# Kernel optimization log

Measured on AMD Instinct MI355X. Metric: run time of the kernel, lower is better.

The kernel has to match this reference:

```python
import jax, jax.numpy as jnp
import numpy as np

NP, P, H, NB = 14, 16, 12, 6  # n_patches per side, patch size, heads, blocks
HD, EMB, SEQ = 64, 768, NP * NP + 1


def _layernorm(x, g, b, eps=1e-5):
    m = x.mean(axis=-1, keepdims=True)
    v = x.var(axis=-1, keepdims=True)
    return (x - m) * jax.lax.rsqrt(v + eps) * g + b


def setup_inputs() -> dict:
    key = jax.random.key(0)
    ks = jax.random.split(key, 16)
    s = 0.02
    B = 64
    inp = {
        "images": jax.random.normal(ks[0], (B, 3, 224, 224), jnp.float32),
        "Wmap": jax.random.normal(ks[1], (768, 768), jnp.float32) * s,
        "bmap": jnp.zeros((768,), jnp.float32),
        "cls_tok": jax.random.normal(ks[2], (1, 768), jnp.float32) * s,
        "pos": jax.random.normal(ks[3], (SEQ, 768), jnp.float32) * s,
        "ln1_g": jnp.ones((NB, 768), jnp.float32),
        "ln1_b": jnp.zeros((NB, 768), jnp.float32),
        "Wq": jax.random.normal(ks[4], (NB, H, HD, HD), jnp.float32) * s,
        "bq": jnp.zeros((NB, H, HD), jnp.float32),
        "Wk": jax.random.normal(ks[5], (NB, H, HD, HD), jnp.float32) * s,
        "bk": jnp.zeros((NB, H, HD), jnp.float32),
        "Wv": jax.random.normal(ks[6], (NB, H, HD, HD), jnp.float32) * s,
        "bv": jnp.zeros((NB, H, HD), jnp.float32),
        "ln2_g": jnp.ones((NB, 768), jnp.float32),
        "ln2_b": jnp.zeros((NB, 768), jnp.float32),
        "W1": jax.random.normal(ks[7], (NB, 768, 3072), jnp.float32) * s,
        "b1": jnp.zeros((NB, 3072), jnp.float32),
        "W2": jax.random.normal(ks[8], (NB, 3072, 768), jnp.float32) * s,
        "b2": jnp.zeros((NB, 768), jnp.float32),
        "Whead": jax.random.normal(ks[9], (768, 10), jnp.float32) * s,
        "bhead": jnp.zeros((10,), jnp.float32),
    }
    return inp


def reference(images, Wmap, bmap, cls_tok, pos, ln1_g, ln1_b, Wq, bq, Wk, bk,
              Wv, bv, ln2_g, ln2_b, W1, b1, W2, b2, Whead, bhead):
    B = images.shape[0]
    # patchify: (B,3,224,224) -> (B,196,768); per-patch channel-first flatten
    x = images.reshape(B, 3, NP, P, NP, P)
    x = x.transpose(0, 2, 4, 1, 3, 5).reshape(B, NP * NP, 3 * P * P)
    tokens = x @ Wmap + bmap  # (B,196,768)
    tokens = jnp.concatenate(
        [jnp.broadcast_to(cls_tok[None], (B, 1, EMB)), tokens], axis=1)
    out = tokens + pos[None]  # (B,197,768)
    scale = 1.0 / jnp.sqrt(jnp.asarray(H, out.dtype))  # NOTE: source divides by sqrt(num_heads)
    for i in range(NB):
        h = _layernorm(out, ln1_g[i], ln1_b[i])
        xh = h.reshape(B, SEQ, H, HD)
        q = jnp.einsum('bshd,hde->bshe', xh, Wq[i]) + bq[i]
        k = jnp.einsum('bshd,hde->bshe', xh, Wk[i]) + bk[i]
        v = jnp.einsum('bshd,hde->bshe', xh, Wv[i]) + bv[i]
        attn = jax.nn.softmax(
            jnp.einsum('bqhd,bkhd->bhqk', q, k) * scale, axis=-1)
        o = jnp.einsum('bhqk,bkhd->bqhd', attn, v).reshape(B, SEQ, EMB)
        out = out + o
        h2 = _layernorm(out, ln2_g[i], ln2_b[i])
        mlp = jax.nn.gelu(h2 @ W1[i] + b1[i], approximate=False) @ W2[i] + b2[i]
        out = out + mlp
    cls = out[:, 0]  # (B,768)
    return jax.nn.softmax(cls @ Whead + bhead, axis=-1)
```

## Files before the change

kernel.cpp:

```cpp
#include <hip/hip_runtime.h>
#include <cstddef>

#define BATCH 64
#define SEQL  197
#define EMB   768
#define NH    12
#define HDIM  64
#define NBLK  6
#define MLPD  3072
#define TOKS  12608
#define PTOK  12544
#define ATT_SCALE 0.28867513459481287f
#define LOG2E 1.4426950408889634f

typedef short bf16x8 __attribute__((ext_vector_type(8)));
typedef float f32x4  __attribute__((ext_vector_type(4)));

__device__ inline float bf2f(unsigned short u) {
  union { unsigned int i; float f; } c; c.i = ((unsigned int)u) << 16; return c.f;
}
__device__ inline unsigned short f2bf(float f) {
  union { float f; unsigned int i; } c; c.f = f;
  unsigned int r = c.i + 0x7FFFu + ((c.i >> 16) & 1u);
  return (unsigned short)(r >> 16);
}

__device__ __forceinline__ float gelu_f(float x) {
  float u = __builtin_fabsf(x) * 0.70710678118654752f;
  float t = __builtin_amdgcn_rcpf(__builtin_fmaf(0.3275911f, u, 1.0f));
  float p = __builtin_fmaf(1.061405429f, t, -1.453152027f);
  p = __builtin_fmaf(p, t, 1.421413741f);
  p = __builtin_fmaf(p, t, -0.284496736f);
  p = __builtin_fmaf(p, t, 0.254829592f);
  p = p * t;
  float e = __expf(-u * u);
  float er = __builtin_fmaf(-p, e, 1.0f);
  er = __builtin_copysignf(er, x);
  return 0.5f * x * (1.0f + er);
}

__device__ __forceinline__ void gload16(const unsigned short* g, void* l) {
  __builtin_amdgcn_global_load_lds(
      (const __attribute__((address_space(1))) unsigned int*)g,
      (__attribute__((address_space(3))) unsigned int*)l, 16, 0, 0);
}

__global__ __launch_bounds__(256) void patchify_kernel(const float* __restrict__ img,
                                                       unsigned short* __restrict__ out) {
  int i4 = blockIdx.x * 256 + threadIdx.x;
  int f4 = i4 % 192;
  int r  = i4 / 192;
  int b  = r / 196, t = r - b * 196;
  int f  = f4 * 4;
  int c  = f >> 8;
  int rem = f & 255;
  int iy = rem >> 4, ix = rem & 15;
  int py = t / 14, px = t - py * 14;
  const float* src = img + ((((size_t)b * 3 + c) * 224 + py * 16 + iy) * 224 + px * 16 + ix);
  float4 v = *(const float4*)src;
  ushort4 u;
  u.x = f2bf(v.x); u.y = f2bf(v.y); u.z = f2bf(v.z); u.w = f2bf(v.w);
  *(ushort4*)(out + (size_t)r * 768 + f) = u;
}

__global__ __launch_bounds__(256) void clspos_kernel(const float* __restrict__ cls,
                                                     const float* __restrict__ pos,
                                                     float* __restrict__ X) {
  int idx = blockIdx.x * 256 + threadIdx.x;
  int b = idx / 768, e = idx - b * 768;
  X[(size_t)b * SEQL * 768 + e] = cls[e] + pos[e];
}

__global__ __launch_bounds__(256) void wconv_kernel(const float* __restrict__ W,
                                                    unsigned short* __restrict__ Wt,
                                                    int K, int N, int perm) {
  __shared__ float t[32][33];
  int k0 = blockIdx.x * 32, n0 = blockIdx.y * 32;
  int kk = threadIdx.x >> 3, nn = (threadIdx.x & 7) * 4;
  float4 v = *(const float4*)&W[(size_t)(k0 + kk) * N + n0 + nn];
  t[nn + 0][kk] = v.x; t[nn + 1][kk] = v.y; t[nn + 2][kk] = v.z; t[nn + 3][kk] = v.w;
  __syncthreads();
  int nr = threadIdx.x >> 3, kc = (threadIdx.x & 7) * 4;
  ushort4 u;
  u.x = f2bf(t[nr][kc + 0]); u.y = f2bf(t[nr][kc + 1]);
  u.z = f2bf(t[nr][kc + 2]); u.w = f2bf(t[nr][kc + 3]);
  if (!perm) {
    *(ushort4*)&Wt[(size_t)(n0 + nr) * K + k0 + kc] = u;
  } else {
    size_t base = (size_t)(n0 + nr) * K + (size_t)(k0 & ~63);
    int klo = (k0 & 32) + kc;
    size_t st = base + (size_t)((klo & 15) * 4 + (klo >> 4));
    Wt[st + 0]  = u.x;
    Wt[st + 4]  = u.y;
    Wt[st + 8]  = u.z;
    Wt[st + 12] = u.w;
  }
}

__global__ __launch_bounds__(256) void qwconv_kernel(const float* __restrict__ Wq,
                                                     const float* __restrict__ Wk,
                                                     const float* __restrict__ Wv,
                                                     unsigned short* __restrict__ Wt) {
  int mh = blockIdx.x;
  int m = mh / 12, h = mh - m * 12;
  const float* src = (m == 0 ? Wq : (m == 1 ? Wk : Wv)) + (size_t)h * 4096;
  unsigned short* dst = Wt + (size_t)mh * 4096;
  for (int idx = threadIdx.x; idx < 4096; idx += 256) {
    int d = idx >> 6, e = idx & 63;
    dst[e * 64 + d] = f2bf(src[idx]);
  }
}

template<int MODE>
__global__ __launch_bounds__(256) void gemm_mfma(const unsigned short* __restrict__ A, int lda,
                                                 const unsigned short* __restrict__ Bt, int ldb,
                                                 void* __restrict__ Cv,
                                                 const float* __restrict__ bias,
                                                 const float* __restrict__ pos,
                                                 int M, int N, int K) {
  __shared__ short As[8192];
  __shared__ short Bs[8192];
  const int tid  = threadIdx.x;
  const int wid  = tid >> 6, lane = tid & 63;
  const int wr   = wid >> 1, wc = wid & 1;
  const int fr   = lane & 15;
  const int fq   = lane >> 4;
  const int m0   = blockIdx.y * 128;
  const int n0   = blockIdx.x * 128;
  const int srow = lane >> 3;
  const int schk = lane & 7;
  const int Mc   = M - 1;

  f32x4 acc[4][4];
#pragma unroll
  for (int m = 0; m < 4; ++m)
#pragma unroll
    for (int n = 0; n < 4; ++n) acc[m][n] = (f32x4)0.f;

  for (int k0 = 0; k0 < K; k0 += 64) {
#pragma unroll
    for (int i = 0; i < 4; ++i) {
      int row = i * 32 + wid * 8 + srow;
      int gr = m0 + row; if (gr > Mc) gr = Mc;
      gload16(A + (size_t)gr * lda + k0 + ((schk ^ (row & 7)) << 3),
              (char*)As + i * 4096 + wid * 1024);
      gload16(Bt + (size_t)(n0 + row) * ldb + k0 + ((schk ^ (row & 7)) << 3),
              (char*)Bs + i * 4096 + wid * 1024);
    }
    __syncthreads();
#pragma unroll
    for (int ks = 0; ks < 2; ++ks) {
      bf16x8 af[4], bfr[4];
#pragma unroll
      for (int m = 0; m < 4; ++m) {
        int row = (wr << 6) + (m << 4) + fr;
        int ch = ((ks << 2) + fq) ^ (row & 7);
        af[m] = *(const bf16x8*)&As[(row << 6) + (ch << 3)];
      }
#pragma unroll
      for (int n = 0; n < 4; ++n) {
        int row = (wc << 6) + (n << 4) + fr;
        int ch = ((ks << 2) + fq) ^ (row & 7);
        bfr[n] = *(const bf16x8*)&Bs[(row << 6) + (ch << 3)];
      }
#pragma unroll
      for (int m = 0; m < 4; ++m)
#pragma unroll
        for (int n = 0; n < 4; ++n)
          acc[m][n] = __builtin_amdgcn_mfma_f32_16x16x32_bf16(af[m], bfr[n], acc[m][n], 0, 0, 0);
    }
    __syncthreads();
  }

#pragma unroll
  for (int m = 0; m < 4; ++m) {
#pragma unroll
    for (int j = 0; j < 4; ++j) {
      int r = m0 + (wr << 6) + (m << 4) + (fq << 2) + j;
      if (r >= M) continue;
      if (MODE == 1) {
        ushort4 q;
        float v0 = acc[m][0][j] + bias[n0 + (wc << 6) + 0 * 16 + fr];
        float v1 = acc[m][1][j] + bias[n0 + (wc << 6) + 1 * 16 + fr];
        float v2 = acc[m][2][j] + bias[n0 + (wc << 6) + 2 * 16 + fr];
        float v3 = acc[m][3][j] + bias[n0 + (wc << 6) + 3 * 16 + fr];
        q.x = f2bf(gelu_f(v0));
        q.y = f2bf(gelu_f(v1));
        q.z = f2bf(gelu_f(v2));
        q.w = f2bf(gelu_f(v3));
        *(ushort4*)&((unsigned short*)Cv)[(size_t)r * MLPD + n0 + (wc << 6) + fr * 4] = q;
      } else {
#pragma unroll
        for (int n = 0; n < 4; ++n) {
          int c = n0 + (wc << 6) + (n << 4) + fr;
          float v = acc[m][n][j] + bias[c];
          if (MODE == 0) {
            int b = r / 196, t = r - b * 196;
            ((float*)Cv)[((size_t)b * SEQL + 1 + t) * 768 + c] = v + pos[(size_t)(1 + t) * 768 + c];
          } else {
            ((float*)Cv)[(size_t)r * 768 + c] += v;
          }
        }
      }
    }
  }
}

__global__ __launch_bounds__(256) void ln_kernel(const float* __restrict__ Xi,
                                                 unsigned short* __restrict__ Ho,
                                                 const float* __restrict__ g,
                                                 const float* __restrict__ bb) {
  int tok = blockIdx.x * 4 + (threadIdx.x >> 6);
  int lane = threadIdx.x & 63;
  const float* x = Xi + (size_t)tok * 768;
  float4 v0 = *(const float4*)(x + lane * 4);
  float4 v1 = *(const float4*)(x + 256 + lane * 4);
  float4 v2 = *(const float4*)(x + 512 + lane * 4);
  float s = v0.x + v0.y + v0.z + v0.w + v1.x + v1.y + v1.z + v1.w + v2.x + v2.y + v2.z + v2.w;
  float q = v0.x*v0.x + v0.y*v0.y + v0.z*v0.z + v0.w*v0.w
          + v1.x*v1.x + v1.y*v1.y + v1.z*v1.z + v1.w*v1.w
          + v2.x*v2.x + v2.y*v2.y + v2.z*v2.z + v2.w*v2.w;
#pragma unroll
  for (int o = 32; o > 0; o >>= 1) { s += __shfl_xor(s, o); q += __shfl_xor(q, o); }
  float mean = s * (1.f / 768.f);
  float var  = q * (1.f / 768.f) - mean * mean;
  float rs = rsqrtf(var + 1e-5f);
  unsigned short* outp = Ho + (size_t)tok * 768;
  float4 g0 = *(const float4*)(g + lane * 4);
  float4 g1 = *(const float4*)(g + 256 + lane * 4);
  float4 g2 = *(const float4*)(g + 512 + lane * 4);
  float4 b0 = *(const float4*)(bb + lane * 4);
  float4 b1 = *(const float4*)(bb + 256 + lane * 4);
  float4 b2 = *(const float4*)(bb + 512 + lane * 4);
  ushort4 s0, s1, s2;
  s0.x = f2bf((v0.x - mean) * rs * g0.x + b0.x); s0.y = f2bf((v0.y - mean) * rs * g0.y + b0.y);
  s0.z = f2bf((v0.z - mean) * rs * g0.z + b0.z); s0.w = f2bf((v0.w - mean) * rs * g0.w + b0.w);
  s1.x = f2bf((v1.x - mean) * rs * g1.x + b1.x); s1.y = f2bf((v1.y - mean) * rs * g1.y + b1.y);
  s1.z = f2bf((v1.z - mean) * rs * g1.z + b1.z); s1.w = f2bf((v1.w - mean) * rs * g1.w + b1.w);
  s2.x = f2bf((v2.x - mean) * rs * g2.x + b2.x); s2.y = f2bf((v2.y - mean) * rs * g2.y + b2.y);
  s2.z = f2bf((v2.z - mean) * rs * g2.z + b2.z); s2.w = f2bf((v2.w - mean) * rs * g2.w + b2.w);
  *(ushort4*)(outp + lane * 4) = s0;
  *(ushort4*)(outp + 256 + lane * 4) = s1;
  *(ushort4*)(outp + 512 + lane * 4) = s2;
}

__global__ __launch_bounds__(256) void qkv_mfma(const unsigned short* __restrict__ Hb,
    const unsigned short* __restrict__ Wt,
    const float* __restrict__ bq, const float* __restrict__ bk, const float* __restrict__ bv,
    unsigned short* __restrict__ Qo, unsigned short* __restrict__ Ko,
    unsigned short* __restrict__ Vo) {
  const int h = blockIdx.y;
  const int tid = threadIdx.x, wv = tid >> 6, lane = tid & 63;
  const int fr = lane & 15, hi = lane >> 4;
  const int t0 = blockIdx.x * 64 + wv * 16;
  const unsigned short* arow = Hb + (size_t)(t0 + fr) * 768 + h * 64;
  bf16x8 a0 = *(const bf16x8*)(arow + hi * 8);
  bf16x8 a1 = *(const bf16x8*)(arow + 32 + hi * 8);
  f32x4 acc[3][4];
#pragma unroll
  for (int m = 0; m < 3; ++m)
#pragma unroll
    for (int n = 0; n < 4; ++n) acc[m][n] = (f32x4)0.f;
#pragma unroll
  for (int m = 0; m < 3; ++m) {
    const unsigned short* wb = Wt + (size_t)(m * 12 + h) * 4096;
#pragma unroll
    for (int n = 0; n < 4; ++n) {
      bf16x8 b0 = *(const bf16x8*)&wb[(n * 16 + fr) * 64 + hi * 8];
      bf16x8 b1 = *(const bf16x8*)&wb[(n * 16 + fr) * 64 + 32 + hi * 8];
      acc[m][n] = __builtin_amdgcn_mfma_f32_16x16x32_bf16(a0, b0, acc[m][n], 0, 0, 0);
      acc[m][n] = __builtin_amdgcn_mfma_f32_16x16x32_bf16(a1, b1, acc[m][n], 0, 0, 0);
    }
  }
#pragma unroll
  for (int m = 0; m < 3; ++m) {
    const float* bptr = (m == 0 ? bq : (m == 1 ? bk : bv)) + h * 64;
    unsigned short* optr = (m == 0 ? Qo : (m == 1 ? Ko : Vo));
    const float sc = (m == 0) ? ATT_SCALE : 1.f;
#pragma unroll
    for (int j = 0; j < 4; ++j) {
      int tk = t0 + hi * 4 + j;
      int b = tk / 197, s = tk - b * 197;
      size_t base_o = (((size_t)b * NH + h) * SEQL + s) * 64;
      if (m < 2) {
        ushort4 o;
        o.x = f2bf((acc[m][0][j] + bptr[0 * 16 + fr]) * sc);
        o.y = f2bf((acc[m][1][j] + bptr[1 * 16 + fr]) * sc);
        o.z = f2bf((acc[m][2][j] + bptr[2 * 16 + fr]) * sc);
        o.w = f2bf((acc[m][3][j] + bptr[3 * 16 + fr]) * sc);
        *(ushort4*)&optr[base_o + fr * 4] = o;
      } else {
#pragma unroll
        for (int n = 0; n < 4; ++n)
          optr[base_o + n * 16 + fr] = f2bf(acc[m][n][j] + bptr[n * 16 + fr]);
      }
    }
  }
}

__global__ __launch_bounds__(256) void attn_kernel(const unsigned short* __restrict__ Q,
                                                   const unsigned short* __restrict__ Kg,
                                                   const unsigned short* __restrict__ Vg,
                                                   float* __restrict__ X) {
  __shared__ unsigned short Vt[64][200];
  __shared__ unsigned short Pl[4][16][200];
  const int bh = blockIdx.x;
  const int b = bh / NH, h = bh - b * NH;
  const int tid = threadIdx.x, wv = tid >> 6, lane = tid & 63;
  const int fr = lane & 15, hi = lane >> 4;
  const unsigned short* Qp = Q  + (size_t)bh * SEQL * 64;
  const unsigned short* Kp = Kg + (size_t)bh * SEQL * 64;
  const unsigned short* Vp = Vg + (size_t)bh * SEQL * 64;

  for (int idx = tid; idx < SEQL * 16; idx += 256) {
    int s = idx >> 4, d4 = (idx & 15) * 4;
    ushort4 v = *(const ushort4*)&Vp[s * 64 + d4];
    Vt[d4 + 0][s] = v.x; Vt[d4 + 1][s] = v.y; Vt[d4 + 2][s] = v.z; Vt[d4 + 3][s] = v.w;
  }
  __syncthreads();

  for (int qt = wv; qt < 13; qt += 4) {
    int qrow = qt * 16 + fr; if (qrow > 196) qrow = 196;
    bf16x8 qa0 = *(const bf16x8*)&Qp[qrow * 64 + hi * 8];
    bf16x8 qa1 = *(const bf16x8*)&Qp[qrow * 64 + 32 + hi * 8];
    f32x4 sc[13];
#pragma unroll
    for (int kt = 0; kt < 13; ++kt) {
      int krow = kt * 16 + fr; if (krow > 196) krow = 196;
      bf16x8 kb0 = *(const bf16x8*)&Kp[krow * 64 + hi * 8];
      bf16x8 kb1 = *(const bf16x8*)&Kp[krow * 64 + 32 + hi * 8];
      f32x4 a = (f32x4)0.f;
      __builtin_amdgcn_s_setprio(1);
      a = __builtin_amdgcn_mfma_f32_16x16x32_bf16(qa0, kb0, a, 0, 0, 0);
      a = __builtin_amdgcn_mfma_f32_16x16x32_bf16(qa1, kb1, a, 0, 0, 0);
      __builtin_amdgcn_s_setprio(0);
      sc[kt] = a;
    }
    float mx[4] = {-3e38f, -3e38f, -3e38f, -3e38f};
#pragma unroll
    for (int kt = 0; kt < 13; ++kt) {
      bool inval = (kt == 12) && (fr >= 5);
#pragma unroll
      for (int j = 0; j < 4; ++j) {
        float s = inval ? -3e38f : sc[kt][j];
        sc[kt][j] = s;
        mx[j] = fmaxf(mx[j], s);
      }
    }
#pragma unroll
    for (int o = 8; o > 0; o >>= 1)
#pragma unroll
      for (int j = 0; j < 4; ++j) mx[j] = fmaxf(mx[j], __shfl_xor(mx[j], o));
    float l[4] = {0.f, 0.f, 0.f, 0.f};
#pragma unroll
    for (int kt = 0; kt < 13; ++kt) {
      int col = kt * 16 + fr;
      bool storev = (col < 200);
#pragma unroll
      for (int j = 0; j < 4; ++j) {
        float p = exp2f((sc[kt][j] - mx[j]) * LOG2E);
        if ((kt == 12) && (fr >= 5)) p = 0.f;
        l[j] += p;
        if (storev) Pl[wv][hi * 4 + j][col] = f2bf(p);
      }
    }
#pragma unroll
    for (int o = 8; o > 0; o >>= 1)
#pragma unroll
      for (int j = 0; j < 4; ++j) l[j] += __shfl_xor(l[j], o);
    f32x4 ov[4];
#pragma unroll
    for (int n = 0; n < 4; ++n) ov[n] = (f32x4)0.f;
#pragma unroll
    for (int kc = 0; kc < 6; ++kc) {
      bf16x8 pa = *(const bf16x8*)&Pl[wv][fr][kc * 32 + hi * 8];
      __builtin_amdgcn_s_setprio(1);
#pragma unroll
      for (int n = 0; n < 4; ++n) {
        bf16x8 vb = *(const bf16x8*)&Vt[n * 16 + fr][kc * 32 + hi * 8];
        ov[n] = __builtin_amdgcn_mfma_f32_16x16x32_bf16(pa, vb, ov[n], 0, 0, 0);
      }
      __builtin_amdgcn_s_setprio(0);
    }
    {
      float pt[4][5];
#pragma unroll
      for (int j = 0; j < 4; ++j) {
        ushort4 p4 = *(ushort4*)&Pl[wv][hi * 4 + j][192];
        unsigned short p5 = Pl[wv][hi * 4 + j][196];
        pt[j][0] = bf2f(p4.x); pt[j][1] = bf2f(p4.y);
        pt[j][2] = bf2f(p4.z); pt[j][3] = bf2f(p4.w); pt[j][4] = bf2f(p5);
      }
#pragma unroll
      for (int n = 0; n < 4; ++n) {
        ushort4 v4 = *(ushort4*)&Vt[n * 16 + fr][192];
        unsigned short v5 = Vt[n * 16 + fr][196];
        float vt[5] = {bf2f(v4.x), bf2f(v4.y), bf2f(v4.z), bf2f(v4.w), bf2f(v5)};
#pragma unroll
        for (int j = 0; j < 4; ++j)
#pragma unroll
          for (int t = 0; t < 5; ++t)
            ov[n][j] = __builtin_fmaf(pt[j][t], vt[t], ov[n][j]);
      }
    }
#pragma unroll
    for (int j = 0; j < 4; ++j) {
      int r = qt * 16 + hi * 4 + j;
      if (r >= SEQL) continue;
      float inv = 1.f / l[j];
      float* xp = X + ((size_t)b * SEQL + r) * 768 + h * 64 + fr;
#pragma unroll
      for (int n = 0; n < 4; ++n) xp[n * 16] += ov[n][j] * inv;
    }
  }
}

__global__ __launch_bounds__(64) void head_kernel(const float* __restrict__ X,
                                                  const float* __restrict__ Wh,
                                                  const float* __restrict__ bh,
                                                  float* __restrict__ out) {
  __shared__ float lg[10];
  int b = blockIdx.x, t = threadIdx.x;
  if (t < 10) {
    float acc = bh[t];
    const float* x = X + (size_t)b * SEQL * 768;
    for (int d = 0; d < 768; ++d) acc += x[d] * Wh[d * 10 + t];
    lg[t] = acc;
  }
  __syncthreads();
  if (t == 0) {
    float m = lg[0];
    for (int c = 1; c < 10; ++c) m = fmaxf(m, lg[c]);
    float ssum = 0.f;
    for (int c = 0; c < 10; ++c) ssum += expf(lg[c] - m);
    for (int c = 0; c < 10; ++c) out[b * 10 + c] = expf(lg[c] - m) / ssum;
  }
}

extern "C" void kernel_launch(void* const* d_in, const int* in_sizes, int n_in,
                              void* d_out, int out_size, void* d_ws, size_t ws_size,
                              hipStream_t stream) {
  const float* images = (const float*)d_in[0];
  const float* Wmap = (const float*)d_in[1];
  const float* bmap = (const float*)d_in[2];
  const float* cls  = (const float*)d_in[3];
  const float* pos  = (const float*)d_in[4];
  const float* ln1g = (const float*)d_in[5];
  const float* ln1b = (const float*)d_in[6];
  const float* Wq   = (const float*)d_in[7];
  const float* bq   = (const float*)d_in[8];
  const float* Wk   = (const float*)d_in[9];
  const float* bk   = (const float*)d_in[10];
  const float* Wv   = (const float*)d_in[11];
  const float* bv   = (const float*)d_in[12];
  const float* ln2g = (const float*)d_in[13];
  const float* ln2b = (const float*)d_in[14];
  const float* W1   = (const float*)d_in[15];
  const float* b1   = (const float*)d_in[16];
  const float* W2   = (const float*)d_in[17];
  const float* b2   = (const float*)d_in[18];
  const float* Wh   = (const float*)d_in[19];
  const float* bhd  = (const float*)d_in[20];
  float* out = (float*)d_out;

  const size_t ACT = (size_t)TOKS * 768;
  const size_t oX = 0;
  const size_t oHb = oX + ACT * 4;
  const size_t oR  = oHb + ACT * 2;
  const size_t oW1 = oR + 3 * ACT * 4;
  const size_t oW2 = oW1 + (size_t)768 * 3072 * 2;
  const size_t oWm = oW2 + (size_t)768 * 3072 * 2;
  const size_t oQW = oWm + (size_t)768 * 768 * 2;
  const size_t need = oQW + (size_t)36 * 4096 * 2;
  if (ws_size < need) return;

  char* ws = (char*)d_ws;
  float* X = (float*)(ws + oX);
  unsigned short* Hb = (unsigned short*)(ws + oHb);
  unsigned short* Qb = (unsigned short*)(ws + oR);
  unsigned short* Kb = Qb + ACT;
  unsigned short* Vb = Kb + ACT;
  unsigned short* mid = (unsigned short*)(ws + oR);
  unsigned short* patches = (unsigned short*)(ws + oR);
  unsigned short* W1t = (unsigned short*)(ws + oW1);
  unsigned short* W2t = (unsigned short*)(ws + oW2);
  unsigned short* Wmapt = (unsigned short*)(ws + oWm);
  unsigned short* QWt = (unsigned short*)(ws + oQW);

  wconv_kernel<<<dim3(24, 24), 256, 0, stream>>>(Wmap, Wmapt, 768, 768, 0);
  patchify_kernel<<<9408, 256, 0, stream>>>(images, patches);
  clspos_kernel<<<192, 256, 0, stream>>>(cls, pos, X);
  gemm_mfma<0><<<dim3(6, 98), 256, 0, stream>>>(patches, 768, Wmapt, 768, X, bmap, pos,
                                                PTOK, 768, 768);

  for (int i = 0; i < NBLK; ++i) {
    ln_kernel<<<3152, 256, 0, stream>>>(X, Hb, ln1g + i * 768, ln1b + i * 768);
    qwconv_kernel<<<36, 256, 0, stream>>>(Wq + (size_t)i * 49152, Wk + (size_t)i * 49152,
                                          Wv + (size_t)i * 49152, QWt);
    qkv_mfma<<<dim3(197, 12), 256, 0, stream>>>(Hb, QWt,
        bq + i * 768, bk + i * 768, bv + i * 768, Qb, Kb, Vb);
    attn_kernel<<<768, 256, 0, stream>>>(Qb, Kb, Vb, X);
    ln_kernel<<<3152, 256, 0, stream>>>(X, Hb, ln2g + i * 768, ln2b + i * 768);
    wconv_kernel<<<dim3(24, 96), 256, 0, stream>>>(W1 + (size_t)i * 2359296, W1t, 768, MLPD, 0);
    wconv_kernel<<<dim3(96, 24), 256, 0, stream>>>(W2 + (size_t)i * 2359296, W2t, MLPD, 768, 1);
    gemm_mfma<1><<<dim3(24, 99), 256, 0, stream>>>(Hb, 768, W1t, 768, mid, b1 + i * MLPD,
                                                   nullptr, TOKS, MLPD, 768);
    gemm_mfma<2><<<dim3(6, 99), 256, 0, stream>>>(mid, MLPD, W2t, MLPD, X, b2 + i * 768,
                                                  nullptr, TOKS, 768, MLPD);
  }
  head_kernel<<<64, 64, 0, stream>>>(X, Wh, bhd, out);
}
```

Before: 1.932 ms.

## Fuse attention residual into LN2, hoist GEMM address math, drop setprio

The attention kernel now writes its per-head output as bf16 into a separate buffer instead of doing a read-modify-write of fp32 X. A new ln_res kernel adds that buffer into X and applies layernorm in one pass, replacing the plain ln_kernel. The GEMM loop precomputes its global and LDS load pointers once and advances them each k-step, and the attention MFMA s_setprio hints are removed. Rounding the attention output to bf16 before the residual add lowers precision slightly, and the extra buffer sits past the Q/K/V region of the workspace.

After: 1.926 ms. No clear change (-0.3%).

```diff
diff --git a/kernel.cpp b/kernel.cpp
--- a/kernel.cpp
+++ b/kernel.cpp
@@ -131,21 +131,35 @@
   const int schk = lane & 7;
   const int Mc   = M - 1;
 
+  const unsigned short* ap[4];
+  const unsigned short* bp[4];
+  char* al[4];
+  char* bl[4];
+#pragma unroll
+  for (int i = 0; i < 4; ++i) {
+    int row = i * 32 + wid * 8 + srow;
+    int gr = m0 + row; if (gr > Mc) gr = Mc;
+    int sw = (schk ^ (row & 7)) << 3;
+    ap[i] = A + (size_t)gr * lda + sw;
+    bp[i] = Bt + (size_t)(n0 + row) * ldb + sw;
+    al[i] = (char*)As + i * 4096 + wid * 1024;
+    bl[i] = (char*)Bs + i * 4096 + wid * 1024;
+  }
+
   f32x4 acc[4][4];
 #pragma unroll
   for (int m = 0; m < 4; ++m)
 #pragma unroll
     for (int n = 0; n < 4; ++n) acc[m][n] = (f32x4)0.f;
 
-  for (int k0 = 0; k0 < K; k0 += 64) {
+  const int T = K >> 6;
+  for (int t = 0; t < T; ++t) {
 #pragma unroll
     for (int i = 0; i < 4; ++i) {
-      int row = i * 32 + wid * 8 + srow;
-      int gr = m0 + row; if (gr > Mc) gr = Mc;
-      gload16(A + (size_t)gr * lda + k0 + ((schk ^ (row & 7)) << 3),
-              (char*)As + i * 4096 + wid * 1024);
-      gload16(Bt + (size_t)(n0 + row) * ldb + k0 + ((schk ^ (row & 7)) << 3),
-              (char*)Bs + i * 4096 + wid * 1024);
+      gload16(ap[i], al[i]);
+      gload16(bp[i], bl[i]);
+      ap[i] += 64;
+      bp[i] += 64;
     }
     __syncthreads();
 #pragma unroll
@@ -244,6 +258,55 @@
   *(ushort4*)(outp + 512 + lane * 4) = s2;
 }
 
+__global__ __launch_bounds__(256) void ln_res_kernel(float* __restrict__ X,
+                                                     const unsigned short* __restrict__ O,
+                                                     unsigned short* __restrict__ Ho,
+                                                     const float* __restrict__ g,
+                                                     const float* __restrict__ bb) {
+  int tok = blockIdx.x * 4 + (threadIdx.x >> 6);
+  int lane = threadIdx.x & 63;
+  float* x = X + (size_t)tok * 768;
+  const unsigned short* op = O + (size_t)tok * 768;
+  float4 v0 = *(const float4*)(x + lane * 4);
+  float4 v1 = *(const float4*)(x + 256 + lane * 4);
+  float4 v2 = *(const float4*)(x + 512 + lane * 4);
+  ushort4 o0 = *(const ushort4*)(op + lane * 4);
+  ushort4 o1 = *(const ushort4*)(op + 256 + lane * 4);
+  ushort4 o2 = *(const ushort4*)(op + 512 + lane * 4);
+  v0.x += bf2f(o0.x); v0.y += bf2f(o0.y); v0.z += bf2f(o0.z); v0.w += bf2f(o0.w);
+  v1.x += bf2f(o1.x); v1.y += bf2f(o1.y); v1.z += bf2f(o1.z); v1.w += bf2f(o1.w);
+  v2.x += bf2f(o2.x); v2.y += bf2f(o2.y); v2.z += bf2f(o2.z); v2.w += bf2f(o2.w);
+  *(float4*)(x + lane * 4) = v0;
+  *(float4*)(x + 256 + lane * 4) = v1;
+  *(float4*)(x + 512 + lane * 4) = v2;
+  float s = v0.x + v0.y + v0.z + v0.w + v1.x + v1.y + v1.z + v1.w + v2.x + v2.y + v2.z + v2.w;
+  float q = v0.x*v0.x + v0.y*v0.y + v0.z*v0.z + v0.w*v0.w
+          + v1.x*v1.x + v1.y*v1.y + v1.z*v1.z + v1.w*v1.w
+          + v2.x*v2.x + v2.y*v2.y + v2.z*v2.z + v2.w*v2.w;
+#pragma unroll
+  for (int o = 32; o > 0; o >>= 1) { s += __shfl_xor(s, o); q += __shfl_xor(q, o); }
+  float mean = s * (1.f / 768.f);
+  float var  = q * (1.f / 768.f) - mean * mean;
+  float rs = rsqrtf(var + 1e-5f);
+  unsigned short* outp = Ho + (size_t)tok * 768;
+  float4 g0 = *(const float4*)(g + lane * 4);
+  float4 g1 = *(const float4*)(g + 256 + lane * 4);
+  float4 g2 = *(const float4*)(g + 512 + lane * 4);
+  float4 b0 = *(const float4*)(bb + lane * 4);
+  float4 b1 = *(const float4*)(bb + 256 + lane * 4);
+  float4 b2 = *(const float4*)(bb + 512 + lane * 4);
+  ushort4 s0, s1, s2;
+  s0.x = f2bf((v0.x - mean) * rs * g0.x + b0.x); s0.y = f2bf((v0.y - mean) * rs * g0.y + b0.y);
+  s0.z = f2bf((v0.z - mean) * rs * g0.z + b0.z); s0.w = f2bf((v0.w - mean) * rs * g0.w + b0.w);
+  s1.x = f2bf((v1.x - mean) * rs * g1.x + b1.x); s1.y = f2bf((v1.y - mean) * rs * g1.y + b1.y);
+  s1.z = f2bf((v1.z - mean) * rs * g1.z + b1.z); s1.w = f2bf((v1.w - mean) * rs * g1.w + b1.w);
+  s2.x = f2bf((v2.x - mean) * rs * g2.x + b2.x); s2.y = f2bf((v2.y - mean) * rs * g2.y + b2.y);
+  s2.z = f2bf((v2.z - mean) * rs * g2.z + b2.z); s2.w = f2bf((v2.w - mean) * rs * g2.w + b2.w);
+  *(ushort4*)(outp + lane * 4) = s0;
+  *(ushort4*)(outp + 256 + lane * 4) = s1;
+  *(ushort4*)(outp + 512 + lane * 4) = s2;
+}
+
 __global__ __launch_bounds__(256) void qkv_mfma(const unsigned short* __restrict__ Hb,
     const unsigned short* __restrict__ Wt,
     const float* __restrict__ bq, const float* __restrict__ bk, const float* __restrict__ bv,
@@ -301,7 +364,7 @@
 __global__ __launch_bounds__(256) void attn_kernel(const unsigned short* __restrict__ Q,
                                                    const unsigned short* __restrict__ Kg,
                                                    const unsigned short* __restrict__ Vg,
-                                                   float* __restrict__ X) {
+                                                   unsigned short* __restrict__ Ob) {
   __shared__ unsigned short Vt[64][200];
   __shared__ unsigned short Pl[4][16][200];
   const int bh = blockIdx.x;
@@ -330,10 +393,8 @@
       bf16x8 kb0 = *(const bf16x8*)&Kp[krow * 64 + hi * 8];
       bf16x8 kb1 = *(const bf16x8*)&Kp[krow * 64 + 32 + hi * 8];
       f32x4 a = (f32x4)0.f;
-      __builtin_amdgcn_s_setprio(1);
       a = __builtin_amdgcn_mfma_f32_16x16x32_bf16(qa0, kb0, a, 0, 0, 0);
       a = __builtin_amdgcn_mfma_f32_16x16x32_bf16(qa1, kb1, a, 0, 0, 0);
-      __builtin_amdgcn_s_setprio(0);
       sc[kt] = a;
     }
     float mx[4] = {-3e38f, -3e38f, -3e38f, -3e38f};
@@ -374,13 +435,11 @@
 #pragma unroll
     for (int kc = 0; kc < 6; ++kc) {
       bf16x8 pa = *(const bf16x8*)&Pl[wv][fr][kc * 32 + hi * 8];
-      __builtin_amdgcn_s_setprio(1);
 #pragma unroll
       for (int n = 0; n < 4; ++n) {
         bf16x8 vb = *(const bf16x8*)&Vt[n * 16 + fr][kc * 32 + hi * 8];
         ov[n] = __builtin_amdgcn_mfma_f32_16x16x32_bf16(pa, vb, ov[n], 0, 0, 0);
       }
-      __builtin_amdgcn_s_setprio(0);
     }
     {
       float pt[4][5];
@@ -408,9 +467,9 @@
       int r = qt * 16 + hi * 4 + j;
       if (r >= SEQL) continue;
       float inv = 1.f / l[j];
-      float* xp = X + ((size_t)b * SEQL + r) * 768 + h * 64 + fr;
-#pragma unroll
-      for (int n = 0; n < 4; ++n) xp[n * 16] += ov[n][j] * inv;
+      unsigned short* op = Ob + ((size_t)b * SEQL + r) * 768 + h * 64 + fr;
+#pragma unroll
+      for (int n = 0; n < 4; ++n) op[n * 16] = f2bf(ov[n][j] * inv);
     }
   }
 }
@@ -481,6 +540,7 @@
   unsigned short* Kb = Qb + ACT;
   unsigned short* Vb = Kb + ACT;
   unsigned short* mid = (unsigned short*)(ws + oR);
+  unsigned short* Obuf = (unsigned short*)(ws + oR + 3 * ACT * 2);
   unsigned short* patches = (unsigned short*)(ws + oR);
   unsigned short* W1t = (unsigned short*)(ws + oW1);
   unsigned short* W2t = (unsigned short*)(ws + oW2);
@@ -499,8 +559,8 @@
                                           Wv + (size_t)i * 49152, QWt);
     qkv_mfma<<<dim3(197, 12), 256, 0, stream>>>(Hb, QWt,
         bq + i * 768, bk + i * 768, bv + i * 768, Qb, Kb, Vb);
-    attn_kernel<<<768, 256, 0, stream>>>(Qb, Kb, Vb, X);
-    ln_kernel<<<3152, 256, 0, stream>>>(X, Hb, ln2g + i * 768, ln2b + i * 768);
+    attn_kernel<<<768, 256, 0, stream>>>(Qb, Kb, Vb, Obuf);
+    ln_res_kernel<<<3152, 256, 0, stream>>>(X, Obuf, Hb, ln2g + i * 768, ln2b + i * 768);
     wconv_kernel<<<dim3(24, 96), 256, 0, stream>>>(W1 + (size_t)i * 2359296, W1t, 768, MLPD, 0);
     wconv_kernel<<<dim3(96, 24), 256, 0, stream>>>(W2 + (size_t)i * 2359296, W2t, MLPD, 768, 1);
     gemm_mfma<1><<<dim3(24, 99), 256, 0, stream>>>(Hb, 768, W1t, 768, mid, b1 + i * MLPD,
```
